# Kernel tuning notes

Measured on AMD Instinct MI355X. Metric: run time of the kernel, lower is better.

The kernel has to match this reference:

```python
import jax, jax.numpy as jnp
import numpy as np

NBINS = 256  # skimage threshold_otsu default
SMOOTH = 1.0


def _otsu_threshold(x):
    """Otsu threshold of a flat float array, skimage-style 256-bin histogram."""
    x = x.reshape(-1)
    xmin = x.min()
    xmax = x.max()
    span = xmax - xmin
    scale = jnp.where(span > 0, NBINS / span, 0.0)
    idx = jnp.clip(((x - xmin) * scale).astype(jnp.int32), 0, NBINS - 1)
    hist = jnp.zeros(NBINS, dtype=x.dtype).at[idx].add(1.0)
    centers = xmin + (jnp.arange(NBINS, dtype=x.dtype) + 0.5) * (span / NBINS)
    # class weights and means (first bin always contains min, last contains max,
    # so the cumulative sums used below are strictly positive)
    w1 = jnp.cumsum(hist)
    w2 = jnp.cumsum(hist[::-1])
    m1 = jnp.cumsum(hist * centers) / w1
    m2 = (jnp.cumsum((hist * centers)[::-1]) / w2)[::-1]
    w2 = w2[::-1]
    var12 = w1[:-1] * w2[1:] * (m1[:-1] - m2[1:]) ** 2  # inter-class variance
    return centers[jnp.argmax(var12)]


def setup_inputs() -> dict:
    key = jax.random.key(0)
    k1, k2 = jax.random.split(key)
    B, C, H, W = 64, 1, 512, 512
    output = jax.random.normal(k1, (B, C, H, W), dtype=jnp.float32)
    target = (jax.random.uniform(k2, (B, C, H, W)) > 0.5).astype(jnp.float32)
    return {"output": output, "target": target}


def reference(output, target):
    probs = jax.nn.sigmoid(output)                    # [B,C,H,W]
    thresh = jax.vmap(_otsu_threshold)(probs)         # per-sample Otsu, [B]
    binary = (probs > thresh[:, None, None, None]).astype(probs.dtype)
    intersection = (binary * target).sum(axis=(-1, -2))          # [B,C]
    union = (binary + target).sum(axis=(-1, -2)) - intersection  # [B,C]
    iou = (intersection + SMOOTH) / (union + SMOOTH)
    return iou.mean()  # reduction='mean'
```

## Files before the change

kernel.cpp:

```cpp
#include <hip/hip_runtime.h>
#include <cstdint>

static constexpr int BATCH = 64;
static constexpr int NPB   = 512 * 512;
static constexpr int NFB   = 2048;

static constexpr int W_BMIN = 0;
static constexpr int W_BMAX = 8192;
static constexpr int W_PART = 16384;

__device__ __forceinline__ float sigmoidf(float v) {
  if (v >= 0.0f) return 1.0f / (1.0f + expf(-v));
  float e = expf(v);
  return e / (1.0f + e);
}
__device__ __forceinline__ float fsig(float v) {
  return __builtin_amdgcn_rcpf(1.0f + __expf(-v));
}

template <int PBLK>
__global__ __launch_bounds__(256) void k_pass(const float* __restrict__ x,
                                              const float* __restrict__ tg,
                                              uint32_t* __restrict__ ws,
                                              float* __restrict__ out) {
  constexpr int ELB  = NPB / PBLK;
  constexpr int ITER = ELB / 4 / 256;
  __shared__ uint32_t h[2 * NFB];
  const int t = threadIdx.x;
  const int g = blockIdx.x;
  if (g == 0 && t == 0) out[0] = 0.0f;
#pragma unroll
  for (int j = 0; j < 4; ++j)
    reinterpret_cast<uint4*>(h)[t + j * 256] = uint4{0u, 0u, 0u, 0u};
  __syncthreads();

  const int b = g / PBLK;
  const int blk = g % PBLK;
  const size_t base = (size_t)b * NPB + (size_t)blk * ELB;
  const float4* px = reinterpret_cast<const float4*>(x + base);
  const float4* pt = reinterpret_cast<const float4*>(tg + base);

  float mn = INFINITY, mx = -INFINITY;
#pragma unroll 4
  for (int i = 0; i < ITER; ++i) {
    float4 v = px[i * 256 + t];
    float4 w = pt[i * 256 + t];
    mn = fminf(mn, fminf(fminf(v.x, v.y), fminf(v.z, v.w)));
    mx = fmaxf(mx, fmaxf(fmaxf(v.x, v.y), fmaxf(v.z, v.w)));
#define PUT(a, c) { int idx = (int)(fsig(a) * 2048.0f);                   \
                    idx = idx > 2047 ? 2047 : idx;                        \
                    idx += ((c) > 0.5f) ? 2048 : 0;                       \
                    atomicAdd(&h[idx], 1u); }
    PUT(v.x, w.x) PUT(v.y, w.y) PUT(v.z, w.z) PUT(v.w, w.w)
#undef PUT
  }
  for (int off = 32; off; off >>= 1) {
    mn = fminf(mn, __shfl_down(mn, off));
    mx = fmaxf(mx, __shfl_down(mx, off));
  }
  if ((t & 63) == 0) {
    float* wsf = reinterpret_cast<float*>(ws);
    wsf[W_BMIN + g * 4 + (t >> 6)] = mn;
    wsf[W_BMAX + g * 4 + (t >> 6)] = mx;
  }
  __syncthreads();
  uint32_t* gp = ws + W_PART + (size_t)g * NFB;
#pragma unroll
  for (int j = 0; j < 8; ++j) {
    const int w = t + j * 256;
    gp[w] = h[2 * w] | (h[2 * w + 1] << 16);
  }
}

template <int PBLK>
__global__ __launch_bounds__(256) void k_finalize(uint32_t* __restrict__ ws,
                                                  float* __restrict__ out) {
  __shared__ uint32_t fj[2 * NFB];
  __shared__ uint32_t h256[256];
  __shared__ uint32_t w1s[256];
  __shared__ float s1s[256];
  __shared__ float vv[256];
  __shared__ int vi[256];
  __shared__ unsigned long long redL[256];
  __shared__ float sPmin, sScale, sBinw;
  const int b = blockIdx.x;
  const int t = threadIdx.x;
  const float* wsf = reinterpret_cast<const float*>(ws);

#pragma unroll
  for (int j = 0; j < 8; ++j) {
    const int w = t + j * 256;
    uint32_t a0 = 0, a1 = 0;
    for (int p = 0; p < PBLK; ++p) {
      const uint32_t v = ws[W_PART + (size_t)(b * PBLK + p) * NFB + w];
      a0 += v & 0xFFFFu;
      a1 += v >> 16;
    }
    fj[2 * w] = a0;
    fj[2 * w + 1] = a1;
  }
  h256[t] = 0u;
  if (t < 64) {
    float mnv = INFINITY, mxv = -INFINITY;
    for (int i = t; i < PBLK * 4; i += 64) {
      mnv = fminf(mnv, wsf[W_BMIN + b * PBLK * 4 + i]);
      mxv = fmaxf(mxv, wsf[W_BMAX + b * PBLK * 4 + i]);
    }
    for (int off = 32; off; off >>= 1) {
      mnv = fminf(mnv, __shfl_down(mnv, off));
      mxv = fmaxf(mxv, __shfl_down(mxv, off));
    }
    if (t == 0) {
      const float pmin = sigmoidf(mnv);
      const float pmax = sigmoidf(mxv);
      const float span = pmax - pmin;
      sPmin = pmin;
      sScale = (span > 0.0f) ? (512.0f / span) : 0.0f;
      sBinw = span * (1.0f / 256.0f);
    }
  }
  __syncthreads();
  const float pmin = sPmin, scale = sScale, binw = sBinw;

#define CIDX(k) ({ const float rep = ((float)(k) + 0.5f) * (1.0f / 2048.0f);  \
                   int ci = (int)((rep - pmin) * scale);                      \
                   ci = ci < 0 ? 0 : (ci > 511 ? 511 : ci); ci; })
#pragma unroll
  for (int j = 0; j < 8; ++j) {
    const int w = t + j * 256;
    const int i0 = 2 * w, i1 = 2 * w + 1;
    const int k0 = i0 & (NFB - 1), k1 = i1 & (NFB - 1);
    if (fj[i0]) atomicAdd(&h256[CIDX(k0) >> 1], fj[i0]);
    if (fj[i1]) atomicAdd(&h256[CIDX(k1) >> 1], fj[i1]);
  }
  __syncthreads();

  const uint32_t hk = h256[t];
  const float ck = pmin + ((float)t + 0.5f) * binw;
  w1s[t] = hk;
  s1s[t] = (float)hk * ck;
  for (int off = 1; off < 256; off <<= 1) {
    __syncthreads();
    uint32_t wp = (t >= off) ? w1s[t - off] : 0u;
    float    sp = (t >= off) ? s1s[t - off] : 0.0f;
    __syncthreads();
    w1s[t] += wp; s1s[t] += sp;
  }
  __syncthreads();
  const uint32_t totW = w1s[255];
  const float totS = s1s[255];
  float v = -INFINITY;
  if (t < 255 && w1s[t] > 0u && totW > w1s[t]) {
    const float w1f = (float)w1s[t];
    const float w2f = (float)(totW - w1s[t]);
    const float m1 = s1s[t] / w1f;
    const float m2 = (totS - s1s[t]) / w2f;
    const float d = m1 - m2;
    v = (w1f * w2f) * (d * d);
  }
  vv[t] = v; vi[t] = t;
  for (int s = 128; s; s >>= 1) {
    __syncthreads();
    if (t < s) {
      const float vb = vv[t + s]; const int ib = vi[t + s];
      if (vb > vv[t] || (vb == vv[t] && ib < vi[t])) { vv[t] = vb; vi[t] = ib; }
    }
  }
  __syncthreads();
  const int J = 2 * vi[0] + 1;

  uint32_t nb_p = 0, ni_p = 0, nt_p = 0;
#pragma unroll
  for (int j = 0; j < 8; ++j) {
    const int w = t + j * 256;
#pragma unroll
    for (int e = 0; e < 2; ++e) {
      const int idx = 2 * w + e;
      const uint32_t cnt = fj[idx];
      const int cls = idx >> 11;
      const int k = idx & (NFB - 1);
      nt_p += cls ? cnt : 0u;
      if (CIDX(k) >= J) { nb_p += cnt; ni_p += cls ? cnt : 0u; }
    }
  }
#undef CIDX
  redL[t] = (unsigned long long)nb_p | ((unsigned long long)ni_p << 20) | ((unsigned long long)nt_p << 40);
  for (int s = 128; s; s >>= 1) {
    __syncthreads();
    if (t < s) redL[t] += redL[t + s];
  }
  __syncthreads();
  if (t == 0) {
    const unsigned long long P = redL[0];
    const float nb = (float)(uint32_t)(P & 0xFFFFFu);
    const float ni = (float)(uint32_t)((P >> 20) & 0xFFFFFu);
    const float nt = (float)(uint32_t)((P >> 40) & 0xFFFFFu);
    const float uni = nb + nt - ni;
    const float iou = (ni + 1.0f) / (uni + 1.0f);
    atomicAdd(out, iou * (1.0f / 64.0f));
  }
}

template <int PBLK>
static void launch_all(const float* x, const float* tg, uint32_t* ws, float* out,
                       hipStream_t stream) {
  hipLaunchKernelGGL((k_pass<PBLK>),     dim3(BATCH * PBLK), dim3(256), 0, stream, x, tg, ws, out);
  hipLaunchKernelGGL((k_finalize<PBLK>), dim3(BATCH),        dim3(256), 0, stream, ws, out);
}

extern "C" void kernel_launch(void* const* d_in, const int* in_sizes, int n_in,
                              void* d_out, int out_size, void* d_ws, size_t ws_size,
                              hipStream_t stream) {
  const float* x  = (const float*)d_in[0];
  const float* tg = (const float*)d_in[1];
  uint32_t* ws = (uint32_t*)d_ws;
  float* out = (float*)d_out;

  const size_t need32 = (size_t)(W_PART + BATCH * 32 * NFB) * 4;
  const size_t need16 = (size_t)(W_PART + BATCH * 16 * NFB) * 4;
  if (ws_size >= need32)      launch_all<32>(x, tg, ws, out, stream);
  else if (ws_size >= need16) launch_all<16>(x, tg, ws, out, stream);
  else                        launch_all<8>(x, tg, ws, out, stream);
}
```

Baseline: 39.02 us.

## Pack total and positive counts into one LDS atomic with per-half-block sub-histograms

Each element now does one workgroup-scoped relaxed atomic add that increments a packed word holding the total count in the low 16 bits and the positive-target count in the high 16 bits, instead of a separate class-indexed bin. The two halves of the block use separate LDS sub-histograms to cut bank and atomic contention, and these are summed when written out. The finalize kernel reads tot/pos arrays directly and the partition count is fixed at 16 blocks per sample, which drops the workspace-size-based dispatch. The 16-bit fields hold the per-block counts safely (16384 elements per block).

```diff
diff --git a/kernel.cpp b/kernel.cpp
--- a/kernel.cpp
+++ b/kernel.cpp
@@ -4,10 +4,12 @@
 static constexpr int BATCH = 64;
 static constexpr int NPB   = 512 * 512;
 static constexpr int NFB   = 2048;
+static constexpr int PBLK  = 16;
+static constexpr int ELB   = NPB / PBLK;
 
 static constexpr int W_BMIN = 0;
-static constexpr int W_BMAX = 8192;
-static constexpr int W_PART = 16384;
+static constexpr int W_BMAX = 4096;
+static constexpr int W_PART = 8192;
 
 __device__ __forceinline__ float sigmoidf(float v) {
   if (v >= 0.0f) return 1.0f / (1.0f + expf(-v));
@@ -18,12 +20,10 @@
   return __builtin_amdgcn_rcpf(1.0f + __expf(-v));
 }
 
-template <int PBLK>
 __global__ __launch_bounds__(256) void k_pass(const float* __restrict__ x,
                                               const float* __restrict__ tg,
                                               uint32_t* __restrict__ ws,
                                               float* __restrict__ out) {
-  constexpr int ELB  = NPB / PBLK;
   constexpr int ITER = ELB / 4 / 256;
   __shared__ uint32_t h[2 * NFB];
   const int t = threadIdx.x;
@@ -34,11 +34,12 @@
     reinterpret_cast<uint4*>(h)[t + j * 256] = uint4{0u, 0u, 0u, 0u};
   __syncthreads();
 
-  const int b = g / PBLK;
-  const int blk = g % PBLK;
+  const int b = g >> 4;
+  const int blk = g & 15;
   const size_t base = (size_t)b * NPB + (size_t)blk * ELB;
   const float4* px = reinterpret_cast<const float4*>(x + base);
   const float4* pt = reinterpret_cast<const float4*>(tg + base);
+  const uint32_t woff = (uint32_t)(t >> 7) << 11;
 
   float mn = INFINITY, mx = -INFINITY;
 #pragma unroll 4
@@ -47,10 +48,11 @@
     float4 w = pt[i * 256 + t];
     mn = fminf(mn, fminf(fminf(v.x, v.y), fminf(v.z, v.w)));
     mx = fmaxf(mx, fmaxf(fmaxf(v.x, v.y), fmaxf(v.z, v.w)));
-#define PUT(a, c) { int idx = (int)(fsig(a) * 2048.0f);                   \
-                    idx = idx > 2047 ? 2047 : idx;                        \
-                    idx += ((c) > 0.5f) ? 2048 : 0;                       \
-                    atomicAdd(&h[idx], 1u); }
+#define PUT(a, c) { int idx = (int)(fsig(a) * 2048.0f);                        \
+                    idx = idx > 2047 ? 2047 : idx;                             \
+                    const uint32_t val = ((c) > 0.5f) ? 0x10001u : 1u;         \
+                    (void)__hip_atomic_fetch_add(&h[woff + idx], val,          \
+                        __ATOMIC_RELAXED, __HIP_MEMORY_SCOPE_WORKGROUP); }
     PUT(v.x, w.x) PUT(v.y, w.y) PUT(v.z, w.z) PUT(v.w, w.w)
 #undef PUT
   }
@@ -68,14 +70,14 @@
 #pragma unroll
   for (int j = 0; j < 8; ++j) {
     const int w = t + j * 256;
-    gp[w] = h[2 * w] | (h[2 * w + 1] << 16);
-  }
-}
-
-template <int PBLK>
+    gp[w] = h[w] + h[w + 2048];
+  }
+}
+
 __global__ __launch_bounds__(256) void k_finalize(uint32_t* __restrict__ ws,
                                                   float* __restrict__ out) {
-  __shared__ uint32_t fj[2 * NFB];
+  __shared__ uint32_t tot[NFB];
+  __shared__ uint32_t pos[NFB];
   __shared__ uint32_t h256[256];
   __shared__ uint32_t w1s[256];
   __shared__ float s1s[256];
@@ -90,14 +92,15 @@
 #pragma unroll
   for (int j = 0; j < 8; ++j) {
     const int w = t + j * 256;
-    uint32_t a0 = 0, a1 = 0;
+    uint32_t at = 0, ap = 0;
+#pragma unroll
     for (int p = 0; p < PBLK; ++p) {
       const uint32_t v = ws[W_PART + (size_t)(b * PBLK + p) * NFB + w];
-      a0 += v & 0xFFFFu;
-      a1 += v >> 16;
-    }
-    fj[2 * w] = a0;
-    fj[2 * w + 1] = a1;
+      at += v & 0xFFFFu;
+      ap += v >> 16;
+    }
+    tot[w] = at;
+    pos[w] = ap;
   }
   h256[t] = 0u;
   if (t < 64) {
@@ -127,11 +130,8 @@
                    ci = ci < 0 ? 0 : (ci > 511 ? 511 : ci); ci; })
 #pragma unroll
   for (int j = 0; j < 8; ++j) {
-    const int w = t + j * 256;
-    const int i0 = 2 * w, i1 = 2 * w + 1;
-    const int k0 = i0 & (NFB - 1), k1 = i1 & (NFB - 1);
-    if (fj[i0]) atomicAdd(&h256[CIDX(k0) >> 1], fj[i0]);
-    if (fj[i1]) atomicAdd(&h256[CIDX(k1) >> 1], fj[i1]);
+    const int k = t + j * 256;
+    if (tot[k]) atomicAdd(&h256[CIDX(k) >> 1], tot[k]);
   }
   __syncthreads();
 
@@ -172,16 +172,10 @@
   uint32_t nb_p = 0, ni_p = 0, nt_p = 0;
 #pragma unroll
   for (int j = 0; j < 8; ++j) {
-    const int w = t + j * 256;
-#pragma unroll
-    for (int e = 0; e < 2; ++e) {
-      const int idx = 2 * w + e;
-      const uint32_t cnt = fj[idx];
-      const int cls = idx >> 11;
-      const int k = idx & (NFB - 1);
-      nt_p += cls ? cnt : 0u;
-      if (CIDX(k) >= J) { nb_p += cnt; ni_p += cls ? cnt : 0u; }
-    }
+    const int k = t + j * 256;
+    const uint32_t ct = tot[k], cp = pos[k];
+    nt_p += cp;
+    if (CIDX(k) >= J) { nb_p += ct; ni_p += cp; }
   }
 #undef CIDX
   redL[t] = (unsigned long long)nb_p | ((unsigned long long)ni_p << 20) | ((unsigned long long)nt_p << 40);
@@ -201,13 +195,6 @@
   }
 }
 
-template <int PBLK>
-static void launch_all(const float* x, const float* tg, uint32_t* ws, float* out,
-                       hipStream_t stream) {
-  hipLaunchKernelGGL((k_pass<PBLK>),     dim3(BATCH * PBLK), dim3(256), 0, stream, x, tg, ws, out);
-  hipLaunchKernelGGL((k_finalize<PBLK>), dim3(BATCH),        dim3(256), 0, stream, ws, out);
-}
-
 extern "C" void kernel_launch(void* const* d_in, const int* in_sizes, int n_in,
                               void* d_out, int out_size, void* d_ws, size_t ws_size,
                               hipStream_t stream) {
@@ -216,9 +203,6 @@
   uint32_t* ws = (uint32_t*)d_ws;
   float* out = (float*)d_out;
 
-  const size_t need32 = (size_t)(W_PART + BATCH * 32 * NFB) * 4;
-  const size_t need16 = (size_t)(W_PART + BATCH * 16 * NFB) * 4;
-  if (ws_size >= need32)      launch_all<32>(x, tg, ws, out, stream);
-  else if (ws_size >= need16) launch_all<16>(x, tg, ws, out, stream);
-  else                        launch_all<8>(x, tg, ws, out, stream);
-}
+  hipLaunchKernelGGL(k_pass,     dim3(BATCH * PBLK), dim3(256), 0, stream, x, tg, ws, out);
+  hipLaunchKernelGGL(k_finalize, dim3(BATCH),        dim3(256), 0, stream, ws, out);
+}
```

After: 35.05 us. 10.2% less time.
